# Kernel optimization log

Hardware: AMD Instinct MI355X
Metric: run time of the kernel (lower is better)

Reference implementation:

```python
import jax, jax.numpy as jnp
import numpy as np

B, N, D = 1, 512, 128


def setup_inputs() -> dict:
    key = jax.random.key(0)
    ks = jax.random.split(key, 8)
    h = jax.random.normal(ks[0], (B, N, D), dtype=jnp.float32)
    rel_emb = jax.random.normal(ks[1], (B, N, N, D), dtype=jnp.float32)
    edge_mask = jax.random.bernoulli(ks[2], 0.5, (B, N, N))
    s2d = 1.0 / np.sqrt(2 * D)
    s1d = 1.0 / np.sqrt(D)
    return {
        "h": h,
        "rel_emb": rel_emb,
        "edge_mask": edge_mask,
        "msg_w1": jax.random.normal(ks[3], (2 * D, D), dtype=jnp.float32) * s2d,
        "msg_b1": jnp.zeros((D,), jnp.float32),
        "msg_w2": jax.random.normal(ks[4], (D, D), dtype=jnp.float32) * s1d,
        "msg_b2": jnp.zeros((D,), jnp.float32),
        "upd_w1": jax.random.normal(ks[5], (2 * D, D), dtype=jnp.float32) * s2d,
        "upd_b1": jnp.zeros((D,), jnp.float32),
        "upd_w2": jax.random.normal(ks[6], (D, D), dtype=jnp.float32) * s1d,
        "upd_b2": jnp.zeros((D,), jnp.float32),
        "ln_g": jnp.ones((D,), jnp.float32),
        "ln_b": jnp.zeros((D,), jnp.float32),
    }


def _layernorm(x, g, b, eps=1e-5):
    mu = x.mean(-1, keepdims=True)
    var = x.var(-1, keepdims=True)
    return (x - mu) * jax.lax.rsqrt(var + eps) * g + b


def reference(h, rel_emb, edge_mask, msg_w1, msg_b1, msg_w2, msg_b2,
              upd_w1, upd_b1, upd_w2, upd_b2, ln_g, ln_b):
    _, n, d = h.shape
    # msg_in = cat([h_j, e_ji]); h_j[b,i,j] = h[b,j], e_ji[b,i,j] = rel_emb[b,j,i]
    # Split first linear so the h-dependent part is computed once per sender j.
    w1_h, w1_e = msg_w1[:d], msg_w1[d:]
    hj_part = h @ w1_h                                   # [B,N,D], indexed by sender j
    e_ji = jnp.swapaxes(rel_emb, 1, 2)                   # [B,N(i),N(j),D]
    pre = hj_part[:, None, :, :] + jnp.einsum('bijd,de->bije', e_ji, w1_e) + msg_b1
    msgs = jax.nn.silu(pre) @ msg_w2 + msg_b2            # [B,N,N,D]
    mask = jnp.swapaxes(edge_mask, 1, 2).astype(h.dtype)  # [B,N(i),N(j)]
    agg = jnp.einsum('bijd,bij->bid', msgs, mask)        # masked sum over senders j
    upd_in = jnp.concatenate([h, agg], axis=-1)          # [B,N,2D]
    delta = jax.nn.silu(upd_in @ upd_w1 + upd_b1) @ upd_w2 + upd_b2
    return _layernorm(h + delta, ln_g, ln_b)
```

## Files before the change

kernel.cpp:

```cpp
#include <hip/hip_runtime.h>
#include <hip/hip_bf16.h>

#define NN 512
#define DD 128

typedef __bf16 bf16x8 __attribute__((ext_vector_type(8)));
typedef float f32x4 __attribute__((ext_vector_type(4)));

static __device__ __forceinline__ f32x4 mfma16(bf16x8 a, bf16x8 b, f32x4 c) {
  return __builtin_amdgcn_mfma_f32_16x16x32_bf16(a, b, c, 0, 0, 0);
}

__global__ void k_pre(const float* __restrict__ h,
                      const float* __restrict__ msg_w1,
                      const float* __restrict__ msg_b1,
                      const int* __restrict__ emask,
                      __bf16* __restrict__ w1t, float* __restrict__ hjp,
                      float* __restrict__ cnt) {
  __shared__ float hr[128];
  __shared__ int csum;
  int j = blockIdx.x, t = threadIdx.x;
  if (t == 0) csum = 0;
  hr[t] = h[j * 128 + t];
  __syncthreads();
  float a0 = msg_b1[t], a1 = 0.f;
  #pragma unroll 16
  for (int k = 0; k < 128; k += 2) {
    a0 += hr[k] * msg_w1[k * 128 + t];
    a1 += hr[k + 1] * msg_w1[(k + 1) * 128 + t];
  }
  hjp[j * 128 + t] = a0 + a1;
  if (t < 32) {
    int tt = j * 32 + t;
    int e = tt >> 7, k = tt & 127;
    w1t[e * 128 + k] = (__bf16)msg_w1[(128 + k) * 128 + e];
  }
  int s = 0;
  #pragma unroll
  for (int r = 0; r < 4; r++) s += emask[(t * 4 + r) * NN + j] ? 1 : 0;
  #pragma unroll
  for (int off = 32; off > 0; off >>= 1) s += __shfl_down(s, off, 64);
  if ((t & 63) == 0) atomicAdd(&csum, s);
  __syncthreads();
  if (t == 0) cnt[j] = (float)csum;
}

#define CVT(bf, xa, xb) { \
  bf[0] = (__bf16)xa[0]; bf[1] = (__bf16)xa[1]; \
  bf[2] = (__bf16)xa[2]; bf[3] = (__bf16)xa[3]; \
  bf[4] = (__bf16)xb[0]; bf[5] = (__bf16)xb[1]; \
  bf[6] = (__bf16)xb[2]; bf[7] = (__bf16)xb[3]; }

__global__ __launch_bounds__(256, 2) void k_main(
    const float* __restrict__ rel, const int* __restrict__ emask,
    const float* __restrict__ hjp, const __bf16* __restrict__ w1t_g,
    float* __restrict__ partial) {
  __shared__ __align__(16) __bf16 tile[2 * 16 * 136];
  __shared__ float mk[256];
  __shared__ __align__(16) float hjl[16 * 128];
  const int tid = threadIdx.x;
  const int wave = tid >> 6;
  const int lane = tid & 63;
  const int l15 = lane & 15;
  const int q = lane >> 4;

  const int it = blockIdx.x >> 5;
  const int jc = blockIdx.x & 31;
  const int irow = it * 16;
  const int jbase = jc * 16;

  mk[tid] = emask[(size_t)(jbase + (tid >> 4)) * NN + irow + (tid & 15)] ? 1.f : 0.f;
  {
    int r2 = tid >> 4, c8 = (tid & 15) * 8;
    const float* hsrc = hjp + (size_t)(jbase + r2) * DD + c8;
    *(f32x4*)(hjl + r2 * 128 + c8) = *(const f32x4*)hsrc;
    *(f32x4*)(hjl + r2 * 128 + c8 + 4) = *(const f32x4*)(hsrc + 4);
  }

  bf16x8 aw00, aw01, aw02, aw03, aw10, aw11, aw12, aw13;
  {
    const __bf16* b0 = w1t_g + (wave * 32 + l15) * 128 + q * 8;
    aw00 = *(const bf16x8*)(b0);
    aw01 = *(const bf16x8*)(b0 + 32);
    aw02 = *(const bf16x8*)(b0 + 64);
    aw03 = *(const bf16x8*)(b0 + 96);
    const __bf16* b1 = b0 + 16 * 128;
    aw10 = *(const bf16x8*)(b1);
    aw11 = *(const bf16x8*)(b1 + 32);
    aw12 = *(const bf16x8*)(b1 + 64);
    aw13 = *(const bf16x8*)(b1 + 96);
  }

  f32x4 t0 = {0.f, 0.f, 0.f, 0.f}, t1 = t0;

  const int srow = tid >> 4;
  const int schunk = tid & 15;
  const float* sb = rel + ((size_t)jbase * NN + irow + srow) * DD + schunk * 8;
  __bf16* sd = tile + srow * 136 + schunk * 8;

  __syncthreads();

  f32x4 xa0 = {0.f, 0.f, 0.f, 0.f}, xb0 = xa0;
  f32x4 xa1 = xa0, xb1 = xa0;
  f32x4 xa2 = xa0, xb2 = xa0;
  f32x4 xa3 = xa0, xb3 = xa0;
  {
    f32x4 ra = xa0, rb = xa0;
    if (mk[srow] != 0.f) { ra = *(const f32x4*)sb; rb = *(const f32x4*)(sb + 4); }
    bf16x8 pub;
    CVT(pub, ra, rb)
    *(bf16x8*)sd = pub;
    if (mk[16 + srow] != 0.f) {
      const float* s = sb + (size_t)NN * DD;
      xa0 = *(const f32x4*)s; xb0 = *(const f32x4*)(s + 4);
    }
    if (mk[32 + srow] != 0.f) {
      const float* s = sb + 2 * (size_t)NN * DD;
      xa1 = *(const f32x4*)s; xb1 = *(const f32x4*)(s + 4);
    }
    if (mk[48 + srow] != 0.f) {
      const float* s = sb + 3 * (size_t)NN * DD;
      xa2 = *(const f32x4*)s; xb2 = *(const f32x4*)(s + 4);
    }
    if (mk[64 + srow] != 0.f) {
      const float* s = sb + 4 * (size_t)NN * DD;
      xa3 = *(const f32x4*)s; xb3 = *(const f32x4*)(s + 4);
    }
  }

  #define COMPUTE(JROW) { \
    const float ms = mk[(JROW) * 16 + l15]; \
    const __bf16* tp = tile + (((JROW) & 1) ? 2176 : 0) + l15 * 136 + q * 8; \
    bf16x8 bf0 = *(const bf16x8*)(tp); \
    bf16x8 bf1 = *(const bf16x8*)(tp + 32); \
    bf16x8 bf2 = *(const bf16x8*)(tp + 64); \
    bf16x8 bf3 = *(const bf16x8*)(tp + 96); \
    f32x4 p0 = {0.f, 0.f, 0.f, 0.f}, p1 = p0; \
    p0 = mfma16(aw00, bf0, p0); p1 = mfma16(aw10, bf0, p1); \
    p0 = mfma16(aw01, bf1, p0); p1 = mfma16(aw11, bf1, p1); \
    p0 = mfma16(aw02, bf2, p0); p1 = mfma16(aw12, bf2, p1); \
    p0 = mfma16(aw03, bf3, p0); p1 = mfma16(aw13, bf3, p1); \
    const float* hj = hjl + (JROW) * 128 + wave * 32 + q * 4; \
    f32x4 hv0 = *(const f32x4*)(hj); \
    f32x4 hv1 = *(const f32x4*)(hj + 16); \
    _Pragma("unroll") \
    for (int r = 0; r < 4; r++) { \
      float v0 = p0[r] + hv0[r]; \
      float v1 = p1[r] + hv1[r]; \
      t0[r] += ms * v0 * __builtin_amdgcn_rcpf(1.f + __expf(-v0)); \
      t1[r] += ms * v1 * __builtin_amdgcn_rcpf(1.f + __expf(-v1)); \
    } }

  #define STEP(JR, XA, XB) { \
    __syncthreads(); \
    if ((JR) + 1 < 16) { \
      bf16x8 pub; \
      CVT(pub, XA, XB) \
      *(bf16x8*)(sd + ((((JR) + 1) & 1) ? 2176 : 0)) = pub; \
    } \
    if ((JR) + 5 < 16) { \
      if (mk[((JR) + 5) * 16 + srow] != 0.f) { \
        const float* s = sb + (size_t)((JR) + 5) * NN * DD; \
        XA = *(const f32x4*)s; XB = *(const f32x4*)(s + 4); \
      } \
    } \
    COMPUTE(JR) }

  #pragma unroll 1
  for (int jj = 0; jj < 16; jj += 4) {
    STEP(jj,     xa0, xb0)
    STEP(jj + 1, xa1, xb1)
    STEP(jj + 2, xa2, xb2)
    STEP(jj + 3, xa3, xb3)
  }
  #undef STEP
  #undef COMPUTE

  float* pp = partial + ((size_t)jc * NN + irow + l15) * DD + wave * 32 + q * 4;
  *(f32x4*)pp = t0;
  *(f32x4*)(pp + 16) = t1;
}

__global__ void k_update(const float* __restrict__ h, const float* __restrict__ partial,
                         const float* __restrict__ w2, const float* __restrict__ b2,
                         const float* __restrict__ cnt,
                         const float* __restrict__ uw1, const float* __restrict__ ub1,
                         const float* __restrict__ uw2, const float* __restrict__ ub2,
                         const float* __restrict__ g, const float* __restrict__ bb,
                         float* __restrict__ out) {
  __shared__ float Trow[128];
  __shared__ float uin[256];
  __shared__ float zl[128];
  __shared__ float ss[4];
  int i = blockIdx.x, t = threadIdx.x;
  float hv = h[i * 128 + t];
  float ts = 0.f;
  #pragma unroll
  for (int c = 0; c < 32; c++) ts += partial[((size_t)c * NN + i) * DD + t];
  Trow[t] = ts;
  __syncthreads();
  float a0 = cnt[i] * b2[t], a1 = 0.f;
  #pragma unroll 16
  for (int e = 0; e < 128; e += 2) {
    a0 += Trow[e] * w2[e * 128 + t];
    a1 += Trow[e + 1] * w2[(e + 1) * 128 + t];
  }
  uin[t] = hv;
  uin[128 + t] = a0 + a1;
  __syncthreads();
  float z0 = ub1[t], z1 = 0.f, z2 = 0.f, z3 = 0.f;
  #pragma unroll 16
  for (int k = 0; k < 256; k += 4) {
    z0 += uin[k] * uw1[k * 128 + t];
    z1 += uin[k + 1] * uw1[(k + 1) * 128 + t];
    z2 += uin[k + 2] * uw1[(k + 2) * 128 + t];
    z3 += uin[k + 3] * uw1[(k + 3) * 128 + t];
  }
  float z = (z0 + z1) + (z2 + z3);
  z = z / (1.f + __expf(-z));
  zl[t] = z;
  __syncthreads();
  float d0 = ub2[t], d1 = 0.f;
  #pragma unroll 16
  for (int k = 0; k < 128; k += 2) {
    d0 += zl[k] * uw2[k * 128 + t];
    d1 += zl[k + 1] * uw2[(k + 1) * 128 + t];
  }
  float x = hv + d0 + d1;
  float s1 = x, s2 = x * x;
  #pragma unroll
  for (int off = 32; off > 0; off >>= 1) {
    s1 += __shfl_down(s1, off, 64);
    s2 += __shfl_down(s2, off, 64);
  }
  if ((t & 63) == 0) { ss[(t >> 6) * 2] = s1; ss[(t >> 6) * 2 + 1] = s2; }
  __syncthreads();
  s1 = ss[0] + ss[2];
  s2 = ss[1] + ss[3];
  float mu = s1 * (1.f / 128.f);
  float var = s2 * (1.f / 128.f) - mu * mu;
  out[i * 128 + t] = (x - mu) * rsqrtf(var + 1e-5f) * g[t] + bb[t];
}

extern "C" void kernel_launch(void* const* d_in, const int* in_sizes, int n_in,
                              void* d_out, int out_size, void* d_ws, size_t ws_size,
                              hipStream_t stream) {
  const float* h      = (const float*)d_in[0];
  const float* rel    = (const float*)d_in[1];
  const int*   emask  = (const int*)d_in[2];
  const float* msg_w1 = (const float*)d_in[3];
  const float* msg_b1 = (const float*)d_in[4];
  const float* msg_w2 = (const float*)d_in[5];
  const float* msg_b2 = (const float*)d_in[6];
  const float* upd_w1 = (const float*)d_in[7];
  const float* upd_b1 = (const float*)d_in[8];
  const float* upd_w2 = (const float*)d_in[9];
  const float* upd_b2 = (const float*)d_in[10];
  const float* ln_g   = (const float*)d_in[11];
  const float* ln_b   = (const float*)d_in[12];
  float* out = (float*)d_out;

  char* ws = (char*)d_ws;
  float*  hjp     = (float*)ws;
  __bf16* w1t     = (__bf16*)(ws + 262144);
  float*  cnt     = (float*)(ws + 262144 + 32768);
  float*  partial = (float*)(ws + 262144 + 36864);

  k_pre<<<512, 128, 0, stream>>>(h, msg_w1, msg_b1, emask, w1t, hjp, cnt);
  k_main<<<1024, 256, 0, stream>>>(rel, emask, hjp, w1t, partial);
  k_update<<<512, 128, 0, stream>>>(h, partial, msg_w2, msg_b2, cnt,
                                    upd_w1, upd_b1, upd_w2, upd_b2,
                                    ln_g, ln_b, out);
}
```

Baseline: 43.16 us.

## Process two sender rows per barrier, quad-buffer tile, batch update kernel rows

The main kernel now uses a four-slot shared tile and handles two sender rows per barrier, which halves the number of __syncthreads, and keeps four rows of rel_emb prefetched in registers. The hj bias is loaded straight from global memory as the MFMA accumulator init instead of being staged in LDS and added afterwards. Mask bits are packed into per-thread bitmasks, replacing repeated LDS reads. The update kernel runs four rows per 512-thread block to cut the block count. Costs are more registers and LDS, which may lower occupancy, and global hjp loads placed inside the compute loop.

```diff
diff --git a/kernel.cpp b/kernel.cpp
--- a/kernel.cpp
+++ b/kernel.cpp
@@ -55,9 +55,8 @@
     const float* __restrict__ rel, const int* __restrict__ emask,
     const float* __restrict__ hjp, const __bf16* __restrict__ w1t_g,
     float* __restrict__ partial) {
-  __shared__ __align__(16) __bf16 tile[2 * 16 * 136];
+  __shared__ __align__(16) __bf16 tile[4 * 16 * 136];
   __shared__ float mk[256];
-  __shared__ __align__(16) float hjl[16 * 128];
   const int tid = threadIdx.x;
   const int wave = tid >> 6;
   const int lane = tid & 63;
@@ -70,12 +69,6 @@
   const int jbase = jc * 16;
 
   mk[tid] = emask[(size_t)(jbase + (tid >> 4)) * NN + irow + (tid & 15)] ? 1.f : 0.f;
-  {
-    int r2 = tid >> 4, c8 = (tid & 15) * 8;
-    const float* hsrc = hjp + (size_t)(jbase + r2) * DD + c8;
-    *(f32x4*)(hjl + r2 * 128 + c8) = *(const f32x4*)hsrc;
-    *(f32x4*)(hjl + r2 * 128 + c8 + 4) = *(const f32x4*)(hsrc + 4);
-  }
 
   bf16x8 aw00, aw01, aw02, aw03, aw10, aw11, aw12, aw13;
   {
@@ -100,78 +93,82 @@
 
   __syncthreads();
 
-  f32x4 xa0 = {0.f, 0.f, 0.f, 0.f}, xb0 = xa0;
-  f32x4 xa1 = xa0, xb1 = xa0;
-  f32x4 xa2 = xa0, xb2 = xa0;
-  f32x4 xa3 = xa0, xb3 = xa0;
+  unsigned msS = 0, msC = 0;
+  #pragma unroll
+  for (int jr = 0; jr < 16; jr++) {
+    msS |= (mk[jr * 16 + srow] != 0.f) ? (1u << jr) : 0u;
+    msC |= (mk[jr * 16 + l15] != 0.f) ? (1u << jr) : 0u;
+  }
+
+  f32x4 Xa0 = {0.f, 0.f, 0.f, 0.f}, Xb0 = Xa0, Xa1 = Xa0, Xb1 = Xa0;
+  f32x4 Ya0 = Xa0, Yb0 = Xa0, Ya1 = Xa0, Yb1 = Xa0;
   {
-    f32x4 ra = xa0, rb = xa0;
-    if (mk[srow] != 0.f) { ra = *(const f32x4*)sb; rb = *(const f32x4*)(sb + 4); }
+    f32x4 ra = Xa0, rb = Xa0;
+    if (msS & 1u) { ra = *(const f32x4*)sb; rb = *(const f32x4*)(sb + 4); }
     bf16x8 pub;
     CVT(pub, ra, rb)
     *(bf16x8*)sd = pub;
-    if (mk[16 + srow] != 0.f) {
+    ra = Xa0; rb = Xa0;
+    if (msS & 2u) {
       const float* s = sb + (size_t)NN * DD;
-      xa0 = *(const f32x4*)s; xb0 = *(const f32x4*)(s + 4);
+      ra = *(const f32x4*)s; rb = *(const f32x4*)(s + 4);
     }
-    if (mk[32 + srow] != 0.f) {
-      const float* s = sb + 2 * (size_t)NN * DD;
-      xa1 = *(const f32x4*)s; xb1 = *(const f32x4*)(s + 4);
-    }
-    if (mk[48 + srow] != 0.f) {
-      const float* s = sb + 3 * (size_t)NN * DD;
-      xa2 = *(const f32x4*)s; xb2 = *(const f32x4*)(s + 4);
-    }
-    if (mk[64 + srow] != 0.f) {
-      const float* s = sb + 4 * (size_t)NN * DD;
-      xa3 = *(const f32x4*)s; xb3 = *(const f32x4*)(s + 4);
-    }
-  }
-
-  #define COMPUTE(JROW) { \
-    const float ms = mk[(JROW) * 16 + l15]; \
-    const __bf16* tp = tile + (((JROW) & 1) ? 2176 : 0) + l15 * 136 + q * 8; \
+    CVT(pub, ra, rb)
+    *(bf16x8*)(sd + 2176) = pub;
+    if (msS & 4u)  { const float* s = sb + 2 * (size_t)NN * DD; Xa0 = *(const f32x4*)s; Xb0 = *(const f32x4*)(s + 4); }
+    if (msS & 8u)  { const float* s = sb + 3 * (size_t)NN * DD; Xa1 = *(const f32x4*)s; Xb1 = *(const f32x4*)(s + 4); }
+    if (msS & 16u) { const float* s = sb + 4 * (size_t)NN * DD; Ya0 = *(const f32x4*)s; Yb0 = *(const f32x4*)(s + 4); }
+    if (msS & 32u) { const float* s = sb + 5 * (size_t)NN * DD; Ya1 = *(const f32x4*)s; Yb1 = *(const f32x4*)(s + 4); }
+  }
+
+  #define COMPUTE(JR) { \
+    const float ms = ((msC >> (JR)) & 1) ? 1.f : 0.f; \
+    const float* hj = hjp + (size_t)(jbase + (JR)) * DD + wave * 32 + q * 4; \
+    f32x4 p0 = *(const f32x4*)(hj); \
+    f32x4 p1 = *(const f32x4*)(hj + 16); \
+    const __bf16* tp = tile + ((JR) & 3) * 2176 + l15 * 136 + q * 8; \
     bf16x8 bf0 = *(const bf16x8*)(tp); \
     bf16x8 bf1 = *(const bf16x8*)(tp + 32); \
     bf16x8 bf2 = *(const bf16x8*)(tp + 64); \
     bf16x8 bf3 = *(const bf16x8*)(tp + 96); \
-    f32x4 p0 = {0.f, 0.f, 0.f, 0.f}, p1 = p0; \
     p0 = mfma16(aw00, bf0, p0); p1 = mfma16(aw10, bf0, p1); \
     p0 = mfma16(aw01, bf1, p0); p1 = mfma16(aw11, bf1, p1); \
     p0 = mfma16(aw02, bf2, p0); p1 = mfma16(aw12, bf2, p1); \
     p0 = mfma16(aw03, bf3, p0); p1 = mfma16(aw13, bf3, p1); \
-    const float* hj = hjl + (JROW) * 128 + wave * 32 + q * 4; \
-    f32x4 hv0 = *(const f32x4*)(hj); \
-    f32x4 hv1 = *(const f32x4*)(hj + 16); \
     _Pragma("unroll") \
     for (int r = 0; r < 4; r++) { \
-      float v0 = p0[r] + hv0[r]; \
-      float v1 = p1[r] + hv1[r]; \
+      float v0 = p0[r]; \
+      float v1 = p1[r]; \
       t0[r] += ms * v0 * __builtin_amdgcn_rcpf(1.f + __expf(-v0)); \
       t1[r] += ms * v1 * __builtin_amdgcn_rcpf(1.f + __expf(-v1)); \
     } }
 
-  #define STEP(JR, XA, XB) { \
+  #define STEP(S, A0, B0, A1, B1) { \
     __syncthreads(); \
-    if ((JR) + 1 < 16) { \
+    if (2 * (S) + 2 < 16) { \
       bf16x8 pub; \
-      CVT(pub, XA, XB) \
-      *(bf16x8*)(sd + ((((JR) + 1) & 1) ? 2176 : 0)) = pub; \
+      CVT(pub, A0, B0) \
+      *(bf16x8*)(sd + ((2 * (S) + 2) & 3) * 2176) = pub; \
+      CVT(pub, A1, B1) \
+      *(bf16x8*)(sd + ((2 * (S) + 3) & 3) * 2176) = pub; \
     } \
-    if ((JR) + 5 < 16) { \
-      if (mk[((JR) + 5) * 16 + srow] != 0.f) { \
-        const float* s = sb + (size_t)((JR) + 5) * NN * DD; \
-        XA = *(const f32x4*)s; XB = *(const f32x4*)(s + 4); \
+    if (2 * (S) + 6 < 16) { \
+      if ((msS >> (2 * (S) + 6)) & 1) { \
+        const float* s = sb + (size_t)(2 * (S) + 6) * NN * DD; \
+        A0 = *(const f32x4*)s; B0 = *(const f32x4*)(s + 4); \
+      } \
+      if ((msS >> (2 * (S) + 7)) & 1) { \
+        const float* s = sb + (size_t)(2 * (S) + 7) * NN * DD; \
+        A1 = *(const f32x4*)s; B1 = *(const f32x4*)(s + 4); \
       } \
     } \
-    COMPUTE(JR) }
+    COMPUTE(2 * (S)) \
+    COMPUTE(2 * (S) + 1) }
 
   #pragma unroll 1
-  for (int jj = 0; jj < 16; jj += 4) {
-    STEP(jj,     xa0, xb0)
-    STEP(jj + 1, xa1, xb1)
-    STEP(jj + 2, xa2, xb2)
-    STEP(jj + 3, xa3, xb3)
+  for (int s2 = 0; s2 < 8; s2 += 2) {
+    STEP(s2,     Xa0, Xb0, Xa1, Xb1)
+    STEP(s2 + 1, Ya0, Yb0, Ya1, Yb1)
   }
   #undef STEP
   #undef COMPUTE
@@ -188,43 +185,44 @@
                          const float* __restrict__ uw2, const float* __restrict__ ub2,
                          const float* __restrict__ g, const float* __restrict__ bb,
                          float* __restrict__ out) {
-  __shared__ float Trow[128];
-  __shared__ float uin[256];
-  __shared__ float zl[128];
-  __shared__ float ss[4];
-  int i = blockIdx.x, t = threadIdx.x;
+  __shared__ float Trow[4][128];
+  __shared__ float uin[4][256];
+  __shared__ float zl[4][128];
+  __shared__ float ss[4][4];
+  int gi = threadIdx.x >> 7, t = threadIdx.x & 127;
+  int i = blockIdx.x * 4 + gi;
   float hv = h[i * 128 + t];
   float ts = 0.f;
   #pragma unroll
   for (int c = 0; c < 32; c++) ts += partial[((size_t)c * NN + i) * DD + t];
-  Trow[t] = ts;
+  Trow[gi][t] = ts;
   __syncthreads();
   float a0 = cnt[i] * b2[t], a1 = 0.f;
   #pragma unroll 16
   for (int e = 0; e < 128; e += 2) {
-    a0 += Trow[e] * w2[e * 128 + t];
-    a1 += Trow[e + 1] * w2[(e + 1) * 128 + t];
-  }
-  uin[t] = hv;
-  uin[128 + t] = a0 + a1;
+    a0 += Trow[gi][e] * w2[e * 128 + t];
+    a1 += Trow[gi][e + 1] * w2[(e + 1) * 128 + t];
+  }
+  uin[gi][t] = hv;
+  uin[gi][128 + t] = a0 + a1;
   __syncthreads();
   float z0 = ub1[t], z1 = 0.f, z2 = 0.f, z3 = 0.f;
   #pragma unroll 16
   for (int k = 0; k < 256; k += 4) {
-    z0 += uin[k] * uw1[k * 128 + t];
-    z1 += uin[k + 1] * uw1[(k + 1) * 128 + t];
-    z2 += uin[k + 2] * uw1[(k + 2) * 128 + t];
-    z3 += uin[k + 3] * uw1[(k + 3) * 128 + t];
+    z0 += uin[gi][k] * uw1[k * 128 + t];
+    z1 += uin[gi][k + 1] * uw1[(k + 1) * 128 + t];
+    z2 += uin[gi][k + 2] * uw1[(k + 2) * 128 + t];
+    z3 += uin[gi][k + 3] * uw1[(k + 3) * 128 + t];
   }
   float z = (z0 + z1) + (z2 + z3);
   z = z / (1.f + __expf(-z));
-  zl[t] = z;
+  zl[gi][t] = z;
   __syncthreads();
   float d0 = ub2[t], d1 = 0.f;
   #pragma unroll 16
   for (int k = 0; k < 128; k += 2) {
-    d0 += zl[k] * uw2[k * 128 + t];
-    d1 += zl[k + 1] * uw2[(k + 1) * 128 + t];
+    d0 += zl[gi][k] * uw2[k * 128 + t];
+    d1 += zl[gi][k + 1] * uw2[(k + 1) * 128 + t];
   }
   float x = hv + d0 + d1;
   float s1 = x, s2 = x * x;
@@ -233,10 +231,10 @@
     s1 += __shfl_down(s1, off, 64);
     s2 += __shfl_down(s2, off, 64);
   }
-  if ((t & 63) == 0) { ss[(t >> 6) * 2] = s1; ss[(t >> 6) * 2 + 1] = s2; }
-  __syncthreads();
-  s1 = ss[0] + ss[2];
-  s2 = ss[1] + ss[3];
+  if ((t & 63) == 0) { ss[gi][(t >> 6) * 2] = s1; ss[gi][(t >> 6) * 2 + 1] = s2; }
+  __syncthreads();
+  s1 = ss[gi][0] + ss[gi][2];
+  s2 = ss[gi][1] + ss[gi][3];
   float mu = s1 * (1.f / 128.f);
   float var = s2 * (1.f / 128.f) - mu * mu;
   out[i * 128 + t] = (x - mu) * rsqrtf(var + 1e-5f) * g[t] + bb[t];
@@ -268,7 +266,7 @@
 
   k_pre<<<512, 128, 0, stream>>>(h, msg_w1, msg_b1, emask, w1t, hjp, cnt);
   k_main<<<1024, 256, 0, stream>>>(rel, emask, hjp, w1t, partial);
-  k_update<<<512, 128, 0, stream>>>(h, partial, msg_w2, msg_b2, cnt,
+  k_update<<<128, 512, 0, stream>>>(h, partial, msg_w2, msg_b2, cnt,
                                     upd_w1, upd_b1, upd_w2, upd_b2,
                                     ln_g, ln_b, out);
 }
```

New measurement: 49.35 us. +14.4%, slower.
